# Kernel optimization log

Measured on AMD Instinct MI355X. Metric: run time of the kernel, lower is better.

## Reference

```python
import jax, jax.numpy as jnp
import numpy as np

B, T, C, H = 2, 2048, 1024, 16
HD = C // H  # head dim = 64


def setup_inputs() -> dict:
    key = jax.random.key(0)
    k1, k2, k3 = jax.random.split(key, 3)
    x = jax.random.normal(k1, (B, T, C), dtype=jnp.float32)
    W_attn = jax.random.normal(k2, (C, 3 * C), dtype=jnp.float32) * (C ** -0.5)
    W_proj = jax.random.normal(k3, (C, C), dtype=jnp.float32) * (C ** -0.5)
    b_proj = jnp.zeros((C,), dtype=jnp.float32)
    return {"x": x, "W_attn": W_attn, "W_proj": W_proj, "b_proj": b_proj}


def reference(x, W_attn, W_proj, b_proj):
    Bv, Tv, Cv = x.shape
    qkv = x @ W_attn  # [B, T, 3C]  (no bias: config.bias=False)
    # NOTE: source splits as k, q, v (k first!)
    k, q, v = jnp.split(qkv, 3, axis=2)
    # [B, H, T, HD]
    q = q.reshape(Bv, Tv, H, HD).transpose(0, 2, 1, 3)
    k = k.reshape(Bv, Tv, H, HD).transpose(0, 2, 1, 3)
    v = v.reshape(Bv, Tv, H, HD).transpose(0, 2, 1, 3)
    wei = jnp.einsum('bhqd,bhkd->bhqk', q, k) * (HD ** -0.5)
    causal = jnp.tril(jnp.ones((Tv, Tv), dtype=bool))
    wei = jnp.where(causal, wei, -jnp.inf)
    wei = jax.nn.softmax(wei, axis=-1)
    # dropout = 0.0 (eval) -> identity
    out = jnp.einsum('bhqk,bhkd->bhqd', wei, v)
    out = out.transpose(0, 2, 1, 3).reshape(Bv, Tv, Cv)
    out = out @ W_proj + b_proj
    return out
```

## Files before the change

### kernel.cpp

```cpp
#include <hip/hip_runtime.h>

typedef __attribute__((ext_vector_type(8))) short short8;
typedef __attribute__((ext_vector_type(4))) short short4v;
typedef __attribute__((ext_vector_type(4))) float float4v;

#define T_SEQ 2048
#define CDIM 1024
#define NHEAD 16
#define HDIM 64
#define LROW 40
#define PROW 72

__device__ __forceinline__ unsigned short f2bf(float f) {
    unsigned u = __builtin_bit_cast(unsigned, f);
    u += 0x7FFF + ((u >> 16) & 1);
    return (unsigned short)(u >> 16);
}

__global__ __launch_bounds__(256) void preproc(
    const float* __restrict__ x, unsigned short* __restrict__ xb,
    const float* __restrict__ Wa, unsigned short* __restrict__ WaT,
    const float* __restrict__ Wp, unsigned short* __restrict__ WpT) {
    int bid = blockIdx.x, tid = threadIdx.x;
    if (bid < 4096) {
        int i = bid * 256 + tid;
        float4 v = ((const float4*)x)[i];
        ushort4 o;
        o.x = f2bf(v.x); o.y = f2bf(v.y); o.z = f2bf(v.z); o.w = f2bf(v.w);
        ((ushort4*)xb)[i] = o;
        return;
    }
    __shared__ float tile[32][33];
    const float* in;
    unsigned short* out;
    int N, b;
    if (bid < 4096 + 3072) {
        b = bid - 4096; in = Wa; out = WaT; N = 3072;
    } else {
        b = bid - 7168; in = Wp; out = WpT; N = 1024;
    }
    const int K = 1024;
    int kb = (b & 31) * 32, nb = (b >> 5) * 32;
    int tx = tid & 31, ty = tid >> 5;
    for (int r = 0; r < 4; r++)
        tile[ty + r * 8][tx] = in[(size_t)(kb + ty + r * 8) * N + nb + tx];
    __syncthreads();
    for (int r = 0; r < 4; r++)
        out[(size_t)(nb + ty + r * 8) * K + kb + tx] = f2bf(tile[tx][ty + r * 8]);
}

__global__ __launch_bounds__(256) void gemm_qkv(
    const unsigned short* __restrict__ A, const unsigned short* __restrict__ Bt,
    unsigned short* __restrict__ dK, unsigned short* __restrict__ dQ,
    unsigned short* __restrict__ dV) {
    const int K = 1024;
    const int NITER = K / 32;
    __shared__ unsigned short sA[2][128 * LROW];
    __shared__ unsigned short sB[2][128 * LROW];
    int tid = threadIdx.x, wave = tid >> 6, lane = tid & 63;
    int quad = lane >> 4, l16 = lane & 15;
    int wm = wave >> 1, wn = wave & 1;
    int blockM = blockIdx.y * 128, blockN = blockIdx.x * 128;
    int rlane = lane >> 2, seg = lane & 3;
    bool swapAB = (blockN >= 2048);

    const unsigned short* gA = A + (size_t)blockM * K;
    const unsigned short* gB = Bt + (size_t)blockN * K;

    float4v acc[4][4] = {};
    uint4 ra[2], rb[2];

    int srow[2], soff[2];
    for (int i = 0; i < 2; i++) {
        srow[i] = wave * 32 + i * 16 + rlane;
        soff[i] = srow[i] * LROW + seg * 8;
    }

    for (int i = 0; i < 2; i++) {
        ra[i] = *(const uint4*)(gA + (size_t)srow[i] * K + seg * 8);
        rb[i] = *(const uint4*)(gB + (size_t)srow[i] * K + seg * 8);
    }
    for (int i = 0; i < 2; i++) {
        *(uint4*)(sA[0] + soff[i]) = ra[i];
        *(uint4*)(sB[0] + soff[i]) = rb[i];
    }

    int aoff = (wm * 64 + l16) * LROW + quad * 8;
    int boff = (wn * 64 + l16) * LROW + quad * 8;

    for (int it = 0; it < NITER; it++) {
        int cur = it & 1;
        __syncthreads();
        if (it + 1 < NITER) {
            int kb = (it + 1) * 32;
            for (int i = 0; i < 2; i++) {
                ra[i] = *(const uint4*)(gA + (size_t)srow[i] * K + kb + seg * 8);
                rb[i] = *(const uint4*)(gB + (size_t)srow[i] * K + kb + seg * 8);
            }
        }
        const unsigned short* cA = sA[cur];
        const unsigned short* cB = sB[cur];
        short8 af[4], bf[4];
        for (int i = 0; i < 4; i++)
            af[i] = *(const short8*)(cA + aoff + i * 16 * LROW);
        for (int j = 0; j < 4; j++)
            bf[j] = *(const short8*)(cB + boff + j * 16 * LROW);
        if (!swapAB) {
            for (int i = 0; i < 4; i++)
                for (int j = 0; j < 4; j++)
                    acc[i][j] = __builtin_amdgcn_mfma_f32_16x16x32_bf16(
                        af[i], bf[j], acc[i][j], 0, 0, 0);
        } else {
            for (int i = 0; i < 4; i++)
                for (int j = 0; j < 4; j++)
                    acc[i][j] = __builtin_amdgcn_mfma_f32_16x16x32_bf16(
                        bf[j], af[i], acc[i][j], 0, 0, 0);
        }
        if (it + 1 < NITER) {
            int nxt = cur ^ 1;
            for (int i = 0; i < 2; i++) {
                *(uint4*)(sA[nxt] + soff[i]) = ra[i];
                *(uint4*)(sB[nxt] + soff[i]) = rb[i];
            }
        }
    }

    if (!swapAB) {
        const float QSCL = 0.18033688011112042f;
        for (int i = 0; i < 4; i++)
            for (int j = 0; j < 4; j++)
                for (int r = 0; r < 4; r++) {
                    int m = blockM + wm * 64 + i * 16 + quad * 4 + r;
                    int n = blockN + wn * 64 + j * 16 + l16;
                    int part = n >> 10, c = n & 1023;
                    int h = c >> 6, d = c & 63;
                    int bb = m >> 11, t = m & 2047;
                    int bh = bb * NHEAD + h;
                    if (part == 0) {
                        dK[(((size_t)bh * T_SEQ + t) << 6) + d] = f2bf(acc[i][j][r]);
                    } else {
                        dQ[(((size_t)bh * T_SEQ + t) << 6) + d] =
                            f2bf(acc[i][j][r] * QSCL);
                    }
                }
    } else {
        for (int i = 0; i < 4; i++)
            for (int j = 0; j < 4; j++)
                for (int r = 0; r < 4; r++) {
                    int n = blockN + wn * 64 + j * 16 + quad * 4 + r;
                    int m = blockM + wm * 64 + i * 16 + l16;
                    int c = n & 1023;
                    int h = c >> 6, d = c & 63;
                    int bb = m >> 11, t = m & 2047;
                    int bh = bb * NHEAD + h;
                    dV[((size_t)bh * HDIM + d) * T_SEQ + t] = f2bf(acc[i][j][r]);
                }
    }
}

__global__ __launch_bounds__(256) void gemm_proj(
    const unsigned short* __restrict__ A, const unsigned short* __restrict__ Bt,
    const float* __restrict__ bias, float* __restrict__ out) {
    const int K = 1024;
    const int NITER = K / 64;
    __shared__ unsigned short sA[2][64 * PROW];
    __shared__ unsigned short sB[2][64 * PROW];
    int tid = threadIdx.x, wave = tid >> 6, lane = tid & 63;
    int quad = lane >> 4, l16 = lane & 15;
    int wm = wave >> 1, wn = wave & 1;
    int blockM = blockIdx.y * 64, blockN = blockIdx.x * 64;

    int srow = tid >> 3;
    int sseg = tid & 7;
    const unsigned short* gA0 = A + (size_t)(blockM + srow) * K + sseg * 8;
    const unsigned short* gA1 = gA0 + (size_t)32 * K;
    const unsigned short* gB0 = Bt + (size_t)(blockN + srow) * K + sseg * 8;
    const unsigned short* gB1 = gB0 + (size_t)32 * K;
    int so0 = srow * PROW + sseg * 8;
    int so1 = (srow + 32) * PROW + sseg * 8;

    float4v acc[2][2] = {};
    uint4 ra0, ra1, rb0, rb1;

    ra0 = *(const uint4*)gA0; ra1 = *(const uint4*)gA1;
    rb0 = *(const uint4*)gB0; rb1 = *(const uint4*)gB1;
    *(uint4*)(sA[0] + so0) = ra0;
    *(uint4*)(sA[0] + so1) = ra1;
    *(uint4*)(sB[0] + so0) = rb0;
    *(uint4*)(sB[0] + so1) = rb1;

    int aoff = (wm * 32 + l16) * PROW + quad * 8;
    int boff = (wn * 32 + l16) * PROW + quad * 8;

    for (int it = 0; it < NITER; it++) {
        int cur = it & 1;
        __syncthreads();
        if (it + 1 < NITER) {
            int kb = (it + 1) * 64;
            ra0 = *(const uint4*)(gA0 + kb); ra1 = *(const uint4*)(gA1 + kb);
            rb0 = *(const uint4*)(gB0 + kb); rb1 = *(const uint4*)(gB1 + kb);
        }
        const unsigned short* cA = sA[cur];
        const unsigned short* cB = sB[cur];
        short8 af[2][2], bf[2][2];
        for (int i = 0; i < 2; i++)
            for (int k = 0; k < 2; k++)
                af[i][k] = *(const short8*)(cA + aoff + i * 16 * PROW + k * 32);
        for (int j = 0; j < 2; j++)
            for (int k = 0; k < 2; k++)
                bf[j][k] = *(const short8*)(cB + boff + j * 16 * PROW + k * 32);
        for (int i = 0; i < 2; i++)
            for (int j = 0; j < 2; j++) {
                acc[i][j] = __builtin_amdgcn_mfma_f32_16x16x32_bf16(
                    af[i][0], bf[j][0], acc[i][j], 0, 0, 0);
                acc[i][j] = __builtin_amdgcn_mfma_f32_16x16x32_bf16(
                    af[i][1], bf[j][1], acc[i][j], 0, 0, 0);
            }
        if (it + 1 < NITER) {
            int nxt = cur ^ 1;
            *(uint4*)(sA[nxt] + so0) = ra0;
            *(uint4*)(sA[nxt] + so1) = ra1;
            *(uint4*)(sB[nxt] + so0) = rb0;
            *(uint4*)(sB[nxt] + so1) = rb1;
        }
    }

    for (int i = 0; i < 2; i++)
        for (int j = 0; j < 2; j++)
            for (int r = 0; r < 4; r++) {
                int m = blockM + wm * 32 + i * 16 + quad * 4 + r;
                int n = blockN + wn * 32 + j * 16 + l16;
                out[(size_t)m * CDIM + n] = acc[i][j][r] + bias[n];
            }
}

__global__ __launch_bounds__(256) void attn_fwd(
    const unsigned short* __restrict__ Qp, const unsigned short* __restrict__ Kp,
    const unsigned short* __restrict__ Vt, unsigned short* __restrict__ att) {
    __shared__ unsigned short sK[2][64 * 72];
    __shared__ unsigned short sV[2][64 * 72];
    int tid = threadIdx.x, wave = tid >> 6, lane = tid & 63;
    int quad = lane >> 4, l16 = lane & 15;
    int bh = blockIdx.x;
    int bb = bh >> 4, h = bh & 15;
    size_t baseQ = (size_t)bh * T_SEQ * HDIM;
    size_t baseV = (size_t)bh * HDIM * T_SEQ;
    int row4 = tid >> 2, seg = tid & 3;

    int xt = 31 - blockIdx.y;
    int qb = xt * 64;
    int qrow = qb + wave * 16 + l16;

    const unsigned short* qr = Qp + baseQ + (size_t)qrow * HDIM;
    short8 qf0 = *(const short8*)(qr + quad * 8);
    short8 qf1 = *(const short8*)(qr + 32 + quad * 8);

    float4v o[4] = {};
    float lsum = 0.f;
    int nt = xt + 1;

    uint4 ka, kb2, va, vb;
    {
        const unsigned short* gk = Kp + baseQ + (size_t)row4 * HDIM + seg * 16;
        const unsigned short* gv = Vt + baseV + (size_t)row4 * T_SEQ + seg * 16;
        ka = *(const uint4*)gk; kb2 = *(const uint4*)(gk + 8);
        va = *(const uint4*)gv; vb = *(const uint4*)(gv + 8);
    }
    *(uint4*)(sK[0] + row4 * 72 + seg * 16) = ka;
    *(uint4*)(sK[0] + row4 * 72 + seg * 16 + 8) = kb2;
    *(uint4*)(sV[0] + row4 * 72 + seg * 16) = va;
    *(uint4*)(sV[0] + row4 * 72 + seg * 16 + 8) = vb;

    for (int t = 0; t < nt; t++) {
        int cur = t & 1;
        __syncthreads();
        if (t + 1 < nt) {
            const unsigned short* gk =
                Kp + baseQ + (size_t)((t + 1) * 64 + row4) * HDIM + seg * 16;
            const unsigned short* gv =
                Vt + baseV + (size_t)row4 * T_SEQ + (t + 1) * 64 + seg * 16;
            ka = *(const uint4*)gk; kb2 = *(const uint4*)(gk + 8);
            va = *(const uint4*)gv; vb = *(const uint4*)(gv + 8);
        }

        const unsigned short* cK = sK[cur];
        const unsigned short* cV = sV[cur];
        float4v s[4];
        for (int sub = 0; sub < 4; sub++) {
            short8 kf0 = *(const short8*)(cK + (sub * 16 + l16) * 72 + quad * 8);
            short8 kf1 =
                *(const short8*)(cK + (sub * 16 + l16) * 72 + 32 + quad * 8);
            float4v z = {};
            z = __builtin_amdgcn_mfma_f32_16x16x32_bf16(kf0, qf0, z, 0, 0, 0);
            z = __builtin_amdgcn_mfma_f32_16x16x32_bf16(kf1, qf1, z, 0, 0, 0);
            s[sub] = z;
        }

        bool need_mask = (t * 64 + 63) > (qb + wave * 16);
        float p[16];
        for (int sub = 0; sub < 4; sub++)
            for (int r = 0; r < 4; r++) {
                float v = s[sub][r];
                if (need_mask) {
                    int kg = t * 64 + sub * 16 + quad * 4 + r;
                    v = (kg <= qrow) ? v : -1e30f;
                }
                p[sub * 4 + r] = v;
            }
        unsigned ub[16];
        for (int i = 0; i < 16; i++) {
            float e = exp2f(p[i] - 16.0f);
            unsigned u = __builtin_bit_cast(unsigned, e) & 0xffff0000u;
            ub[i] = u;
            lsum += __builtin_bit_cast(float, u);
        }

        for (int sub = 0; sub < 4; sub++) {
            unsigned lo = __builtin_amdgcn_perm(ub[sub * 4 + 1], ub[sub * 4 + 0],
                                                0x07060302u);
            unsigned hi = __builtin_amdgcn_perm(ub[sub * 4 + 3], ub[sub * 4 + 2],
                                                0x07060302u);
            uint2 packed = {lo, hi};
            short4v pf = __builtin_bit_cast(short4v, packed);
            for (int dc = 0; dc < 4; dc++) {
                short4v vf = *(const short4v*)(
                    cV + (dc * 16 + l16) * 72 + sub * 16 + quad * 4);
                o[dc] = __builtin_amdgcn_mfma_f32_16x16x16bf16_1k(
                    vf, pf, o[dc], 0, 0, 0);
            }
        }

        if (t + 1 < nt) {
            int nxt = cur ^ 1;
            *(uint4*)(sK[nxt] + row4 * 72 + seg * 16) = ka;
            *(uint4*)(sK[nxt] + row4 * 72 + seg * 16 + 8) = kb2;
            *(uint4*)(sV[nxt] + row4 * 72 + seg * 16) = va;
            *(uint4*)(sV[nxt] + row4 * 72 + seg * 16 + 8) = vb;
        }
    }

    lsum += __shfl_xor(lsum, 16);
    lsum += __shfl_xor(lsum, 32);
    float inv = 1.0f / lsum;

    __syncthreads();
    for (int dc = 0; dc < 4; dc++) {
        short4v ov;
        for (int r = 0; r < 4; r++) ov[r] = (short)f2bf(o[dc][r] * inv);
        *(short4v*)(sK[0] + wave * 1152 + l16 * 72 + dc * 16 + quad * 4) = ov;
    }
    __syncthreads();
    int orow = lane >> 2, oseg = lane & 3;
    uint4 a = *(const uint4*)(sK[0] + wave * 1152 + orow * 72 + oseg * 16);
    uint4 b = *(const uint4*)(sK[0] + wave * 1152 + orow * 72 + oseg * 16 + 8);
    unsigned short* dst = att +
        (size_t)(bb * T_SEQ + qb + wave * 16 + orow) * CDIM + h * HDIM +
        oseg * 16;
    *(uint4*)dst = a;
    *(uint4*)(dst + 8) = b;
}

extern "C" void kernel_launch(void* const* d_in, const int* in_sizes, int n_in,
                              void* d_out, int out_size, void* d_ws, size_t ws_size,
                              hipStream_t stream) {
    const float* x      = (const float*)d_in[0];
    const float* W_attn = (const float*)d_in[1];
    const float* W_proj = (const float*)d_in[2];
    const float* b_proj = (const float*)d_in[3];
    float* out = (float*)d_out;

    unsigned short* xb   = (unsigned short*)d_ws;
    unsigned short* WaT  = xb  + 4096 * 1024;
    unsigned short* WpT  = WaT + 3072 * 1024;
    unsigned short* Karr = WpT + 1024 * 1024;
    unsigned short* Qarr = Karr + 2 * 16 * 2048 * 64;
    unsigned short* Varr = Qarr + 2 * 16 * 2048 * 64;
    unsigned short* attb = Varr + 2 * 16 * 2048 * 64;

    preproc<<<8192, 256, 0, stream>>>(x, xb, W_attn, WaT, W_proj, WpT);
    gemm_qkv<<<dim3(24, 32), 256, 0, stream>>>(xb, WaT, Karr, Qarr, Varr);
    attn_fwd<<<dim3(32, 32), 256, 0, stream>>>(Qarr, Karr, Varr, attb);
    gemm_proj<<<dim3(16, 64), 256, 0, stream>>>(attb, WpT, b_proj, out);
}
```

Measured before the change: 194.1 us.

## Use direct global-to-LDS loads with triple-buffered pipeline in QKV GEMM

Replaces the register-staged double-buffered tile loads in the QKV projection GEMM with global_load_lds direct-to-LDS transfers and a three-stage ring buffer, prefetching two K-tiles ahead with explicit vmcnt waits and raw s_barrier. This removes the VGPR round trip and the LDS store instructions, and lets memory loads overlap more MFMA work. The LDS row padding is dropped (stride 32 instead of 40), which may introduce bank conflicts on the fragment reads. The main loop is also fully unrolled.

```diff
diff --git a/kernel.cpp b/kernel.cpp
--- a/kernel.cpp
+++ b/kernel.cpp
@@ -8,13 +8,25 @@
 #define CDIM 1024
 #define NHEAD 16
 #define HDIM 64
-#define LROW 40
 #define PROW 72
 
 __device__ __forceinline__ unsigned short f2bf(float f) {
     unsigned u = __builtin_bit_cast(unsigned, f);
     u += 0x7FFF + ((u >> 16) & 1);
     return (unsigned short)(u >> 16);
+}
+
+__device__ __forceinline__ void gload16(const unsigned short* g,
+                                        unsigned short* l) {
+    __builtin_amdgcn_global_load_lds(
+        (const __attribute__((address_space(1))) unsigned int*)g,
+        (__attribute__((address_space(3))) unsigned int*)l, 16, 0, 0);
+}
+
+__device__ __forceinline__ void phase_barrier() {
+    __builtin_amdgcn_sched_barrier(0);
+    __builtin_amdgcn_s_barrier();
+    __builtin_amdgcn_sched_barrier(0);
 }
 
 __global__ __launch_bounds__(256) void preproc(
@@ -55,56 +67,58 @@
     unsigned short* __restrict__ dV) {
     const int K = 1024;
     const int NITER = K / 32;
-    __shared__ unsigned short sA[2][128 * LROW];
-    __shared__ unsigned short sB[2][128 * LROW];
+    __shared__ unsigned short sA[3][128 * 32];
+    __shared__ unsigned short sB[3][128 * 32];
     int tid = threadIdx.x, wave = tid >> 6, lane = tid & 63;
     int quad = lane >> 4, l16 = lane & 15;
     int wm = wave >> 1, wn = wave & 1;
     int blockM = blockIdx.y * 128, blockN = blockIdx.x * 128;
-    int rlane = lane >> 2, seg = lane & 3;
     bool swapAB = (blockN >= 2048);
 
     const unsigned short* gA = A + (size_t)blockM * K;
     const unsigned short* gB = Bt + (size_t)blockN * K;
 
+    int srow = wave * 32 + (lane >> 2);
+    int scol = (lane & 3) * 8;
+    const unsigned short* pa0 = gA + (size_t)srow * K + scol;
+    const unsigned short* pa1 = pa0 + (size_t)16 * K;
+    const unsigned short* pb0 = gB + (size_t)srow * K + scol;
+    const unsigned short* pb1 = pb0 + (size_t)16 * K;
+    int lo0 = (wave * 32) * 32;
+    int lo1 = (wave * 32 + 16) * 32;
+
     float4v acc[4][4] = {};
-    uint4 ra[2], rb[2];
-
-    int srow[2], soff[2];
-    for (int i = 0; i < 2; i++) {
-        srow[i] = wave * 32 + i * 16 + rlane;
-        soff[i] = srow[i] * LROW + seg * 8;
-    }
-
-    for (int i = 0; i < 2; i++) {
-        ra[i] = *(const uint4*)(gA + (size_t)srow[i] * K + seg * 8);
-        rb[i] = *(const uint4*)(gB + (size_t)srow[i] * K + seg * 8);
-    }
-    for (int i = 0; i < 2; i++) {
-        *(uint4*)(sA[0] + soff[i]) = ra[i];
-        *(uint4*)(sB[0] + soff[i]) = rb[i];
-    }
-
-    int aoff = (wm * 64 + l16) * LROW + quad * 8;
-    int boff = (wn * 64 + l16) * LROW + quad * 8;
-
+    int aoff = (wm * 64 + l16) * 32 + quad * 8;
+    int boff = (wn * 64 + l16) * 32 + quad * 8;
+
+    for (int t = 0; t < 2; t++) {
+        int kb = t * 32;
+        gload16(pa0 + kb, sA[t] + lo0);
+        gload16(pa1 + kb, sA[t] + lo1);
+        gload16(pb0 + kb, sB[t] + lo0);
+        gload16(pb1 + kb, sB[t] + lo1);
+    }
+    asm volatile("s_waitcnt vmcnt(4)" ::: "memory");
+    phase_barrier();
+
+#pragma unroll
     for (int it = 0; it < NITER; it++) {
-        int cur = it & 1;
-        __syncthreads();
-        if (it + 1 < NITER) {
-            int kb = (it + 1) * 32;
-            for (int i = 0; i < 2; i++) {
-                ra[i] = *(const uint4*)(gA + (size_t)srow[i] * K + kb + seg * 8);
-                rb[i] = *(const uint4*)(gB + (size_t)srow[i] * K + kb + seg * 8);
-            }
+        int cur = it % 3;
+        if (it + 2 < NITER) {
+            int kb = (it + 2) * 32;
+            int nb = (it + 2) % 3;
+            gload16(pa0 + kb, sA[nb] + lo0);
+            gload16(pa1 + kb, sA[nb] + lo1);
+            gload16(pb0 + kb, sB[nb] + lo0);
+            gload16(pb1 + kb, sB[nb] + lo1);
         }
         const unsigned short* cA = sA[cur];
         const unsigned short* cB = sB[cur];
         short8 af[4], bf[4];
         for (int i = 0; i < 4; i++)
-            af[i] = *(const short8*)(cA + aoff + i * 16 * LROW);
+            af[i] = *(const short8*)(cA + aoff + i * 16 * 32);
         for (int j = 0; j < 4; j++)
-            bf[j] = *(const short8*)(cB + boff + j * 16 * LROW);
+            bf[j] = *(const short8*)(cB + boff + j * 16 * 32);
         if (!swapAB) {
             for (int i = 0; i < 4; i++)
                 for (int j = 0; j < 4; j++)
@@ -117,11 +131,12 @@
                         bf[j], af[i], acc[i][j], 0, 0, 0);
         }
         if (it + 1 < NITER) {
-            int nxt = cur ^ 1;
-            for (int i = 0; i < 2; i++) {
-                *(uint4*)(sA[nxt] + soff[i]) = ra[i];
-                *(uint4*)(sB[nxt] + soff[i]) = rb[i];
-            }
+            if (it + 2 < NITER) {
+                asm volatile("s_waitcnt vmcnt(4)" ::: "memory");
+            } else {
+                asm volatile("s_waitcnt vmcnt(0)" ::: "memory");
+            }
+            phase_barrier();
         }
     }
 
```

Result: no change. 190.7 us (-1.7%).
